# Kernel tuning notes

Measured on AMD Instinct MI355X. Metric: run time of the kernel, lower is better.

Reference implementation:

```python
import jax, jax.numpy as jnp
import numpy as np
from jax import lax

WORD_NUM = 30000
EMBED = 128
RNN = 256
CLASSES = 9
BATCH = 128
SEQ = 512


def setup_inputs() -> dict:
    key = jax.random.key(0)
    ks = jax.random.split(key, 7)
    s_e = 1.0 / np.sqrt(EMBED)
    s_r = 1.0 / np.sqrt(RNN)
    return {
        "input_x": jax.random.randint(ks[0], (BATCH, SEQ), 0, WORD_NUM, dtype=jnp.int32),
        "embed": jax.random.normal(ks[1], (WORD_NUM, EMBED), dtype=jnp.float32) * 0.05,
        # LSTM kernel/recurrent kernel, gate order i|f|g|o (Keras convention)
        "W": jax.random.normal(ks[2], (EMBED, 4 * RNN), dtype=jnp.float32) * s_e,
        "U": jax.random.normal(ks[3], (RNN, 4 * RNN), dtype=jnp.float32) * s_r,
        "b": jnp.zeros((4 * RNN,), dtype=jnp.float32),
        "Wout": jax.random.normal(ks[4], (RNN, CLASSES), dtype=jnp.float32) * s_r,
        "bout": jnp.zeros((CLASSES,), dtype=jnp.float32),
    }


def _lstm(xs, W, U, b, h0, c0):
    # xs: [T, B, E] -> hidden sequence [T, B, R], final (h, c)
    def step(carry, x):
        h, c = carry
        z = x @ W + h @ U + b  # [B, 4R]
        i, f, g, o = jnp.split(z, 4, axis=-1)
        i = jax.nn.sigmoid(i)
        f = jax.nn.sigmoid(f)
        g = jnp.tanh(g)
        o = jax.nn.sigmoid(o)
        c = f * c + i * g
        h = o * jnp.tanh(c)
        return (h, c), h

    (h, c), hs = lax.scan(step, (h0, c0), xs)
    return hs, h, c


def reference(input_x, embed, W, U, b, Wout, bout):
    # Embedding lookup: [B, S] -> [B, S, E]
    x = embed[input_x]
    B = x.shape[0]
    R = U.shape[0]
    h0 = jnp.zeros((B, R), dtype=x.dtype)
    c0 = jnp.zeros((B, R), dtype=x.dtype)
    xs = jnp.swapaxes(x, 0, 1)  # [S, B, E] for time-major scan
    hs, h_last, c_last = _lstm(xs, W, U, b, h0, c0)
    hs = jnp.swapaxes(hs, 0, 1)  # [B, S, R]
    probs = jax.nn.softmax(hs @ Wout + bout, axis=-1)  # [B, S, C]
    # Keras return_state -> (sequence_output, last_h, last_c); state=(hc, hs)
    return probs, (h_last, c_last)
```

## Files before the change

kernel.cpp:

```cpp
#include <hip/hip_runtime.h>
#include <math.h>

#define B 128
#define S 512
#define E 128
#define R 256
#define G4 1024

static const size_t HS_FLOATS = 513ull * R * B;
static const size_t C_OFF     = HS_FLOATS;
static const size_t X4_OFF    = C_OFF + (size_t)R * B;
static const size_t WUT_OFF   = X4_OFF + (size_t)S * E * B;
static const size_t WS_FLOATS = WUT_OFF + (size_t)G4 * 384;

#define HOUT_OFF 589824
#define COUT_OFF 622592

__global__ void zero_state(float4* __restrict__ hs0, float4* __restrict__ c4) {
    int i = blockIdx.x * 256 + threadIdx.x;
    float4 z = make_float4(0.f, 0.f, 0.f, 0.f);
    if (i < 8192) hs0[i] = z;
    else          c4[i - 8192] = z;
}

__global__ void gather_x(const int* __restrict__ idx, const float* __restrict__ embed,
                         float4* __restrict__ X4) {
    int t    = blockIdx.x;
    int tid  = threadIdx.x;
    int b    = tid & 127;
    int half = tid >> 7;
    int row  = idx[(size_t)b * S + t];
    const float4* er = (const float4*)embed + (size_t)row * (E / 4);
    size_t xbase = (size_t)t * (E / 4) * B + b;
#pragma unroll
    for (int kk = 0; kk < 16; ++kk) {
        int e4 = half * 16 + kk;
        X4[xbase + (size_t)e4 * B] = er[e4];
    }
}

__global__ void make_wut(const float* __restrict__ W, const float* __restrict__ U,
                         float* __restrict__ WUt) {
    int j = blockIdx.x;
    int s = threadIdx.x;
    float v = (s < E) ? W[(size_t)s * G4 + j] : U[(size_t)(s - E) * G4 + j];
    WUt[(size_t)j * 384 + s] = v;
}

__launch_bounds__(256, 1)
__global__ void lstm_step(const float4* __restrict__ X4, const float* __restrict__ WUt,
                          const float* __restrict__ bias, float* __restrict__ HS,
                          float* __restrict__ cbuf, float* __restrict__ out, int t) {
    __shared__ float partial[2][4][64];
    int lane = threadIdx.x & 63;
    int wid  = __builtin_amdgcn_readfirstlane((int)(threadIdx.x >> 6));
    int k    = wid & 1;
    int rl   = wid >> 1;
    int r    = blockIdx.x * 2 + rl;
    int bg   = blockIdx.y;
    int b    = bg * 64 + lane;

    const float* wu0 = WUt + (size_t)(0 * R + r) * 384;
    const float* wu1 = WUt + (size_t)(1 * R + r) * 384;
    const float* wu2 = WUt + (size_t)(2 * R + r) * 384;
    const float* wu3 = WUt + (size_t)(3 * R + r) * 384;

    float a0, a1, a2, a3;
    if (k == 0) { a0 = bias[r]; a1 = bias[R + r]; a2 = bias[2 * R + r]; a3 = bias[3 * R + r]; }
    else        { a0 = a1 = a2 = a3 = 0.f; }

    const float4* hs_in = (const float4*)HS + (size_t)t * (R / 4) * B + b;

    if (k == 0) {
        const float4* xp = X4 + (size_t)t * (E / 4) * B + b;
#pragma unroll 4
        for (int e4 = 0; e4 < E / 4; ++e4) {
            float4 xv = xp[(size_t)e4 * B];
            int s = e4 * 4;
            a0 += wu0[s] * xv.x; a0 += wu0[s + 1] * xv.y; a0 += wu0[s + 2] * xv.z; a0 += wu0[s + 3] * xv.w;
            a1 += wu1[s] * xv.x; a1 += wu1[s + 1] * xv.y; a1 += wu1[s + 2] * xv.z; a1 += wu1[s + 3] * xv.w;
            a2 += wu2[s] * xv.x; a2 += wu2[s + 1] * xv.y; a2 += wu2[s + 2] * xv.z; a2 += wu2[s + 3] * xv.w;
            a3 += wu3[s] * xv.x; a3 += wu3[s + 1] * xv.y; a3 += wu3[s + 2] * xv.z; a3 += wu3[s + 3] * xv.w;
        }
#pragma unroll 4
        for (int r4 = 0; r4 < 16; ++r4) {
            float4 hv = hs_in[(size_t)r4 * B];
            int s = E + r4 * 4;
            a0 += wu0[s] * hv.x; a0 += wu0[s + 1] * hv.y; a0 += wu0[s + 2] * hv.z; a0 += wu0[s + 3] * hv.w;
            a1 += wu1[s] * hv.x; a1 += wu1[s + 1] * hv.y; a1 += wu1[s + 2] * hv.z; a1 += wu1[s + 3] * hv.w;
            a2 += wu2[s] * hv.x; a2 += wu2[s + 1] * hv.y; a2 += wu2[s + 2] * hv.z; a2 += wu2[s + 3] * hv.w;
            a3 += wu3[s] * hv.x; a3 += wu3[s + 1] * hv.y; a3 += wu3[s + 2] * hv.z; a3 += wu3[s + 3] * hv.w;
        }
    } else {
#pragma unroll 4
        for (int r4 = 16; r4 < 64; ++r4) {
            float4 hv = hs_in[(size_t)r4 * B];
            int s = E + r4 * 4;
            a0 += wu0[s] * hv.x; a0 += wu0[s + 1] * hv.y; a0 += wu0[s + 2] * hv.z; a0 += wu0[s + 3] * hv.w;
            a1 += wu1[s] * hv.x; a1 += wu1[s + 1] * hv.y; a1 += wu1[s + 2] * hv.z; a1 += wu1[s + 3] * hv.w;
            a2 += wu2[s] * hv.x; a2 += wu2[s + 1] * hv.y; a2 += wu2[s + 2] * hv.z; a2 += wu2[s + 3] * hv.w;
            a3 += wu3[s] * hv.x; a3 += wu3[s + 1] * hv.y; a3 += wu3[s + 2] * hv.z; a3 += wu3[s + 3] * hv.w;
        }
        partial[rl][0][lane] = a0;
        partial[rl][1][lane] = a1;
        partial[rl][2][lane] = a2;
        partial[rl][3][lane] = a3;
    }
    __syncthreads();
    if (k == 0) {
        a0 += partial[rl][0][lane];
        a1 += partial[rl][1][lane];
        a2 += partial[rl][2][lane];
        a3 += partial[rl][3][lane];
        float ii = 1.f / (1.f + expf(-a0));
        float ff = 1.f / (1.f + expf(-a1));
        float gg = tanhf(a2);
        float oo = 1.f / (1.f + expf(-a3));
        float cold = cbuf[(size_t)r * B + b];
        float cn = ff * cold + ii * gg;
        float hn = oo * tanhf(cn);
        cbuf[(size_t)r * B + b] = cn;
        HS[((size_t)(t + 1) * (R / 4) + (r >> 2)) * (B * 4) + (size_t)b * 4 + (r & 3)] = hn;
        if (t == S - 1) {
            out[HOUT_OFF + (size_t)b * R + r] = hn;
            out[COUT_OFF + (size_t)b * R + r] = cn;
        }
    }
}

__global__ void out_probs(const float* __restrict__ HS, const float* __restrict__ Wout,
                          const float* __restrict__ bout, float* __restrict__ out) {
    int t    = blockIdx.x;
    int bg   = blockIdx.y;
    int lane = threadIdx.x;
    int b    = bg * 64 + lane;
    float acc[9];
#pragma unroll
    for (int c = 0; c < 9; ++c) acc[c] = bout[c];
    const float4* hp = (const float4*)HS + (size_t)(t + 1) * (R / 4) * B + b;
#pragma unroll 4
    for (int r4 = 0; r4 < R / 4; ++r4) {
        float4 hv = hp[(size_t)r4 * B];
        int r = r4 * 4;
#pragma unroll
        for (int c = 0; c < 9; ++c) {
            acc[c] += hv.x * Wout[(size_t)(r + 0) * 9 + c];
            acc[c] += hv.y * Wout[(size_t)(r + 1) * 9 + c];
            acc[c] += hv.z * Wout[(size_t)(r + 2) * 9 + c];
            acc[c] += hv.w * Wout[(size_t)(r + 3) * 9 + c];
        }
    }
    float m = acc[0];
#pragma unroll
    for (int c = 1; c < 9; ++c) m = fmaxf(m, acc[c]);
    float e[9];
    float sum = 0.f;
#pragma unroll
    for (int c = 0; c < 9; ++c) { e[c] = expf(acc[c] - m); sum += e[c]; }
    float inv = 1.f / sum;
#pragma unroll
    for (int c = 0; c < 9; ++c) out[((size_t)b * S + t) * 9 + c] = e[c] * inv;
}

extern "C" void kernel_launch(void* const* d_in, const int* in_sizes, int n_in,
                              void* d_out, int out_size, void* d_ws, size_t ws_size,
                              hipStream_t stream) {
    const int*   idx   = (const int*)d_in[0];
    const float* embed = (const float*)d_in[1];
    const float* W     = (const float*)d_in[2];
    const float* U     = (const float*)d_in[3];
    const float* bias  = (const float*)d_in[4];
    const float* Wout  = (const float*)d_in[5];
    const float* bout  = (const float*)d_in[6];
    float*       out   = (float*)d_out;
    float*       ws    = (float*)d_ws;

    if (ws_size < WS_FLOATS * sizeof(float)) return;

    float*  HS   = ws;
    float*  cbuf = ws + C_OFF;
    float4* X4   = (float4*)(ws + X4_OFF);
    float*  WUt  = ws + WUT_OFF;

    zero_state<<<64, 256, 0, stream>>>((float4*)HS, (float4*)cbuf);
    gather_x<<<S, 256, 0, stream>>>(idx, embed, X4);
    make_wut<<<G4, 384, 0, stream>>>(W, U, WUt);
    for (int t = 0; t < S; ++t)
        lstm_step<<<dim3(R / 2, 2), 256, 0, stream>>>(X4, WUt, bias, HS, cbuf, out, t);
    out_probs<<<dim3(S, 2), 64, 0, stream>>>(HS, Wout, bout, out);
}
```

Measured before the change: 3.947 ms.

## Replace per-timestep launches with persistent LSTM kernel using hierarchical grid barrier

The 512 per-timestep kernel launches are replaced by one persistent kernel of 256 blocks that loops over time and synchronises through a two-level atomic counter/flag barrier in workspace. The cell state now stays in a register instead of global memory, and each block's reduction is split across four waves instead of two. Hidden-state stores bypass caches so other blocks can see them after the barrier. This removes launch overhead per step, but depends on all blocks being co-resident and adds spin-wait costs; the barrier spin loops have an iteration cap that could silently break correctness if exceeded.

```diff
diff --git a/kernel.cpp b/kernel.cpp
--- a/kernel.cpp
+++ b/kernel.cpp
@@ -7,20 +7,19 @@
 #define R 256
 #define G4 1024
 
-static const size_t HS_FLOATS = 513ull * R * B;
-static const size_t C_OFF     = HS_FLOATS;
-static const size_t X4_OFF    = C_OFF + (size_t)R * B;
-static const size_t WUT_OFF   = X4_OFF + (size_t)S * E * B;
-static const size_t WS_FLOATS = WUT_OFF + (size_t)G4 * 384;
+static const size_t HS_FLOATS = 513ull * (R / 4) * (B * 4);
+static const size_t X4_OFF    = HS_FLOATS;
+static const size_t WUT_OFF   = X4_OFF + (size_t)S * (E / 4) * (B * 4);
+static const size_t SYNC_OFF  = WUT_OFF + (size_t)G4 * 384;
+static const size_t WS_FLOATS = SYNC_OFF + 1024;
 
 #define HOUT_OFF 589824
 #define COUT_OFF 622592
 
-__global__ void zero_state(float4* __restrict__ hs0, float4* __restrict__ c4) {
-    int i = blockIdx.x * 256 + threadIdx.x;
-    float4 z = make_float4(0.f, 0.f, 0.f, 0.f);
-    if (i < 8192) hs0[i] = z;
-    else          c4[i - 8192] = z;
+__global__ void zero_state(float* __restrict__ HS, int* __restrict__ sync) {
+    int i = blockIdx.x * 1024 + threadIdx.x;
+    if (i < 32768) HS[i] = 0.f;
+    if (i < 1024) sync[i] = 0;
 }
 
 __global__ void gather_x(const int* __restrict__ idx, const float* __restrict__ embed,
@@ -47,83 +46,129 @@
     WUt[(size_t)j * 384 + s] = v;
 }
 
-__launch_bounds__(256, 1)
-__global__ void lstm_step(const float4* __restrict__ X4, const float* __restrict__ WUt,
-                          const float* __restrict__ bias, float* __restrict__ HS,
-                          float* __restrict__ cbuf, float* __restrict__ out, int t) {
-    __shared__ float partial[2][4][64];
-    int lane = threadIdx.x & 63;
-    int wid  = __builtin_amdgcn_readfirstlane((int)(threadIdx.x >> 6));
-    int k    = wid & 1;
-    int rl   = wid >> 1;
-    int r    = blockIdx.x * 2 + rl;
-    int bg   = blockIdx.y;
-    int b    = bg * 64 + lane;
+__device__ __forceinline__ float sigmoidf_(float x) { return 1.f / (1.f + __expf(-x)); }
+
+__launch_bounds__(512, 2)
+__global__ void lstm_persist(const float4* __restrict__ X4, const float* __restrict__ WUt,
+                             const float* __restrict__ bias, float* __restrict__ HS,
+                             float* __restrict__ out, int* __restrict__ sync) {
+    const int tid  = threadIdx.x;
+    const int lane = tid & 63;
+    const int wid  = __builtin_amdgcn_readfirstlane((int)(tid >> 6));
+    const int k    = wid & 3;
+    const int rl   = wid >> 2;
+    const int w    = blockIdx.x;
+    const int rpair = w >> 1;
+    const int bg    = w & 1;
+    const int r     = rpair * 2 + rl;
+    const int b     = bg * 64 + lane;
+    const int xg    = w & 7;
+
+    __shared__ float partial[2][3][4][64];
 
     const float* wu0 = WUt + (size_t)(0 * R + r) * 384;
     const float* wu1 = WUt + (size_t)(1 * R + r) * 384;
     const float* wu2 = WUt + (size_t)(2 * R + r) * 384;
     const float* wu3 = WUt + (size_t)(3 * R + r) * 384;
 
-    float a0, a1, a2, a3;
-    if (k == 0) { a0 = bias[r]; a1 = bias[R + r]; a2 = bias[2 * R + r]; a3 = bias[3 * R + r]; }
-    else        { a0 = a1 = a2 = a3 = 0.f; }
-
-    const float4* hs_in = (const float4*)HS + (size_t)t * (R / 4) * B + b;
-
-    if (k == 0) {
-        const float4* xp = X4 + (size_t)t * (E / 4) * B + b;
-#pragma unroll 4
-        for (int e4 = 0; e4 < E / 4; ++e4) {
-            float4 xv = xp[(size_t)e4 * B];
-            int s = e4 * 4;
-            a0 += wu0[s] * xv.x; a0 += wu0[s + 1] * xv.y; a0 += wu0[s + 2] * xv.z; a0 += wu0[s + 3] * xv.w;
-            a1 += wu1[s] * xv.x; a1 += wu1[s + 1] * xv.y; a1 += wu1[s + 2] * xv.z; a1 += wu1[s + 3] * xv.w;
-            a2 += wu2[s] * xv.x; a2 += wu2[s + 1] * xv.y; a2 += wu2[s + 2] * xv.z; a2 += wu2[s + 3] * xv.w;
-            a3 += wu3[s] * xv.x; a3 += wu3[s + 1] * xv.y; a3 += wu3[s + 2] * xv.z; a3 += wu3[s + 3] * xv.w;
-        }
-#pragma unroll 4
-        for (int r4 = 0; r4 < 16; ++r4) {
-            float4 hv = hs_in[(size_t)r4 * B];
-            int s = E + r4 * 4;
-            a0 += wu0[s] * hv.x; a0 += wu0[s + 1] * hv.y; a0 += wu0[s + 2] * hv.z; a0 += wu0[s + 3] * hv.w;
-            a1 += wu1[s] * hv.x; a1 += wu1[s + 1] * hv.y; a1 += wu1[s + 2] * hv.z; a1 += wu1[s + 3] * hv.w;
-            a2 += wu2[s] * hv.x; a2 += wu2[s + 1] * hv.y; a2 += wu2[s + 2] * hv.z; a2 += wu2[s + 3] * hv.w;
-            a3 += wu3[s] * hv.x; a3 += wu3[s + 1] * hv.y; a3 += wu3[s + 2] * hv.z; a3 += wu3[s + 3] * hv.w;
-        }
-    } else {
-#pragma unroll 4
-        for (int r4 = 16; r4 < 64; ++r4) {
-            float4 hv = hs_in[(size_t)r4 * B];
-            int s = E + r4 * 4;
-            a0 += wu0[s] * hv.x; a0 += wu0[s + 1] * hv.y; a0 += wu0[s + 2] * hv.z; a0 += wu0[s + 3] * hv.w;
-            a1 += wu1[s] * hv.x; a1 += wu1[s + 1] * hv.y; a1 += wu1[s + 2] * hv.z; a1 += wu1[s + 3] * hv.w;
-            a2 += wu2[s] * hv.x; a2 += wu2[s + 1] * hv.y; a2 += wu2[s + 2] * hv.z; a2 += wu2[s + 3] * hv.w;
-            a3 += wu3[s] * hv.x; a3 += wu3[s + 1] * hv.y; a3 += wu3[s + 2] * hv.z; a3 += wu3[s + 3] * hv.w;
-        }
-        partial[rl][0][lane] = a0;
-        partial[rl][1][lane] = a1;
-        partial[rl][2][lane] = a2;
-        partial[rl][3][lane] = a3;
-    }
-    __syncthreads();
-    if (k == 0) {
-        a0 += partial[rl][0][lane];
-        a1 += partial[rl][1][lane];
-        a2 += partial[rl][2][lane];
-        a3 += partial[rl][3][lane];
-        float ii = 1.f / (1.f + expf(-a0));
-        float ff = 1.f / (1.f + expf(-a1));
-        float gg = tanhf(a2);
-        float oo = 1.f / (1.f + expf(-a3));
-        float cold = cbuf[(size_t)r * B + b];
-        float cn = ff * cold + ii * gg;
-        float hn = oo * tanhf(cn);
-        cbuf[(size_t)r * B + b] = cn;
-        HS[((size_t)(t + 1) * (R / 4) + (r >> 2)) * (B * 4) + (size_t)b * 4 + (r & 3)] = hn;
-        if (t == S - 1) {
-            out[HOUT_OFF + (size_t)b * R + r] = hn;
-            out[COUT_OFF + (size_t)b * R + r] = cn;
+    int* cnt1 = sync + xg * 64;
+    int* flg1 = sync + 512 + xg * 64;
+    int* cntr = sync + 1016;
+    int* flgr = sync + 1020;
+
+    float c = 0.f;
+
+    for (int t = 0; t < S; ++t) {
+        float a0, a1, a2, a3;
+        if (k == 0) { a0 = bias[r]; a1 = bias[R + r]; a2 = bias[2 * R + r]; a3 = bias[3 * R + r]; }
+        else        { a0 = a1 = a2 = a3 = 0.f; }
+
+        const float4* xp = X4 + (size_t)t * (E / 4) * B;
+        const float4* hp = (const float4*)HS + (size_t)t * (R / 4) * B;
+
+#define MACX(E0, E1)                                                                   \
+        _Pragma("unroll")                                                              \
+        for (int m = (E0); m < (E1); ++m) {                                            \
+            float4 v = xp[(size_t)m * B + b];                                          \
+            int s = m * 4;                                                             \
+            a0 += wu0[s] * v.x; a0 += wu0[s+1] * v.y; a0 += wu0[s+2] * v.z; a0 += wu0[s+3] * v.w; \
+            a1 += wu1[s] * v.x; a1 += wu1[s+1] * v.y; a1 += wu1[s+2] * v.z; a1 += wu1[s+3] * v.w; \
+            a2 += wu2[s] * v.x; a2 += wu2[s+1] * v.y; a2 += wu2[s+2] * v.z; a2 += wu2[s+3] * v.w; \
+            a3 += wu3[s] * v.x; a3 += wu3[s+1] * v.y; a3 += wu3[s+2] * v.z; a3 += wu3[s+3] * v.w; \
+        }
+#define MACH(R0, R1)                                                                   \
+        _Pragma("unroll")                                                              \
+        for (int m = (R0); m < (R1); ++m) {                                            \
+            float4 v = hp[(size_t)m * B + b];                                          \
+            int s = E + m * 4;                                                         \
+            a0 += wu0[s] * v.x; a0 += wu0[s+1] * v.y; a0 += wu0[s+2] * v.z; a0 += wu0[s+3] * v.w; \
+            a1 += wu1[s] * v.x; a1 += wu1[s+1] * v.y; a1 += wu1[s+2] * v.z; a1 += wu1[s+3] * v.w; \
+            a2 += wu2[s] * v.x; a2 += wu2[s+1] * v.y; a2 += wu2[s+2] * v.z; a2 += wu2[s+3] * v.w; \
+            a3 += wu3[s] * v.x; a3 += wu3[s+1] * v.y; a3 += wu3[s+2] * v.z; a3 += wu3[s+3] * v.w; \
+        }
+
+        if (k == 0)      { MACX(0, 24) }
+        else if (k == 1) { MACX(24, 32) MACH(0, 16) }
+        else if (k == 2) { MACH(16, 40) }
+        else             { MACH(40, 64) }
+#undef MACX
+#undef MACH
+
+        if (k != 0) {
+            partial[rl][k - 1][0][lane] = a0;
+            partial[rl][k - 1][1][lane] = a1;
+            partial[rl][k - 1][2][lane] = a2;
+            partial[rl][k - 1][3][lane] = a3;
+        }
+        __syncthreads();
+
+        if (k == 0) {
+#pragma unroll
+            for (int kk = 0; kk < 3; ++kk) {
+                a0 += partial[rl][kk][0][lane];
+                a1 += partial[rl][kk][1][lane];
+                a2 += partial[rl][kk][2][lane];
+                a3 += partial[rl][kk][3][lane];
+            }
+            float ig = sigmoidf_(a0);
+            float fg = sigmoidf_(a1);
+            float gg = tanhf(a2);
+            float og = sigmoidf_(a3);
+            c = fg * c + ig * gg;
+            float h = og * tanhf(c);
+            float* haddr = HS + ((size_t)(t + 1) * (R / 4) + (r >> 2)) * (B * 4) + (size_t)b * 4 + (r & 3);
+            asm volatile("global_store_dword %0, %1, off sc0 sc1" :: "v"(haddr), "v"(h) : "memory");
+            if (t == S - 1) {
+                out[HOUT_OFF + (size_t)b * R + r] = h;
+                out[COUT_OFF + (size_t)b * R + r] = c;
+            }
+        }
+        asm volatile("s_waitcnt vmcnt(0)" ::: "memory");
+        __syncthreads();
+
+        if (t < S - 1) {
+            if (tid == 0) {
+                int epoch = t + 1;
+                int a = __hip_atomic_fetch_add(cnt1, 1, __ATOMIC_ACQ_REL, __HIP_MEMORY_SCOPE_AGENT);
+                if (a == 31) {
+                    __hip_atomic_store(cnt1, 0, __ATOMIC_RELAXED, __HIP_MEMORY_SCOPE_AGENT);
+                    int rr = __hip_atomic_fetch_add(cntr, 1, __ATOMIC_ACQ_REL, __HIP_MEMORY_SCOPE_AGENT);
+                    if (rr == 7) {
+                        __hip_atomic_store(cntr, 0, __ATOMIC_RELAXED, __HIP_MEMORY_SCOPE_AGENT);
+                        __hip_atomic_store(flgr, epoch, __ATOMIC_RELEASE, __HIP_MEMORY_SCOPE_AGENT);
+                    } else {
+                        int it = 0;
+                        while (__hip_atomic_load(flgr, __ATOMIC_RELAXED, __HIP_MEMORY_SCOPE_AGENT) < epoch
+                               && ++it < (1 << 20)) __builtin_amdgcn_s_sleep(2);
+                    }
+                    __hip_atomic_store(flg1, epoch, __ATOMIC_RELEASE, __HIP_MEMORY_SCOPE_AGENT);
+                } else {
+                    int it = 0;
+                    while (__hip_atomic_load(flg1, __ATOMIC_RELAXED, __HIP_MEMORY_SCOPE_AGENT) < epoch
+                           && ++it < (1 << 20)) __builtin_amdgcn_s_sleep(2);
+                }
+            }
+            __syncthreads();
         }
     }
 }
@@ -178,14 +223,13 @@
     if (ws_size < WS_FLOATS * sizeof(float)) return;
 
     float*  HS   = ws;
-    float*  cbuf = ws + C_OFF;
     float4* X4   = (float4*)(ws + X4_OFF);
     float*  WUt  = ws + WUT_OFF;
-
-    zero_state<<<64, 256, 0, stream>>>((float4*)HS, (float4*)cbuf);
+    int*    sync = (int*)(ws + SYNC_OFF);
+
+    zero_state<<<32, 1024, 0, stream>>>(HS, sync);
     gather_x<<<S, 256, 0, stream>>>(idx, embed, X4);
     make_wut<<<G4, 384, 0, stream>>>(W, U, WUt);
-    for (int t = 0; t < S; ++t)
-        lstm_step<<<dim3(R / 2, 2), 256, 0, stream>>>(X4, WUt, bias, HS, cbuf, out, t);
+    lstm_persist<<<256, 512, 0, stream>>>(X4, WUt, bias, HS, out, sync);
     out_probs<<<dim3(S, 2), 64, 0, stream>>>(HS, Wout, bout, out);
 }
```

New measurement: 4.741 ms. +20.1%, slower.
